# Kernel tuning notes

Measured on AMD Instinct MI355X. Metric: run time of the kernel, lower is better.

Reference implementation:

```python
import jax, jax.numpy as jnp
import numpy as np

WIN_H = WIN_W = 7
NUM_HEADS = 6
DIM = 192
HEAD_DIM = DIM // NUM_HEADS
NUM_WIN = 1024
B_ = 8192
N = WIN_H * WIN_W


def _relative_position_index(win_h, win_w):
    coords = np.stack(np.meshgrid(np.arange(win_h), np.arange(win_w), indexing='ij'))  # (2,h,w)
    flat = coords.reshape(2, -1)
    rel = flat[:, :, None] - flat[:, None, :]          # (2, N, N)
    rel = rel.transpose(1, 2, 0).astype(np.int32)      # (N, N, 2)
    rel[:, :, 0] += win_h - 1
    rel[:, :, 1] += win_w - 1
    rel[:, :, 0] *= 2 * win_w - 1
    return rel.sum(-1)                                 # (N, N) in [0, (2h-1)(2w-1))


def setup_inputs() -> dict:
    key = jax.random.key(0)
    ks = jax.random.split(key, 7)
    return {
        'x': jax.random.normal(ks[0], (B_, N, DIM), jnp.float32),
        'mask': jax.random.normal(ks[1], (NUM_WIN, N, N), jnp.float32),
        'qkv_w': jax.random.normal(ks[2], (3 * DIM, DIM), jnp.float32) * 0.02,
        'qkv_b': jax.random.normal(ks[3], (3 * DIM,), jnp.float32) * 0.02,
        'proj_w': jax.random.normal(ks[4], (DIM, DIM), jnp.float32) * 0.02,
        'proj_b': jax.random.normal(ks[5], (DIM,), jnp.float32) * 0.02,
        'rpb_table': jax.random.normal(ks[6], ((2 * WIN_H - 1) * (2 * WIN_W - 1), NUM_HEADS), jnp.float32) * 0.02,
        'rel_index': jnp.asarray(_relative_position_index(WIN_H, WIN_W)),
    }


def reference(x, mask, qkv_w, qkv_b, proj_w, proj_b, rpb_table, rel_index):
    B, n, C = x.shape
    H, hd = NUM_HEADS, HEAD_DIM
    scale = hd ** (-0.5)

    qkv = (x @ qkv_w.T + qkv_b).reshape(B, n, 3, H, hd)
    qkv = jnp.transpose(qkv, (2, 0, 3, 1, 4))          # (3, B, H, N, hd)
    q, k, v = qkv[0], qkv[1], qkv[2]

    attn = jnp.einsum('bhnd,bhmd->bhnm', q * scale, k)  # (B, H, N, N)

    # gathered relative position bias: (N*N,) -> (N, N, H) -> (H, N, N)
    bias = rpb_table[rel_index.reshape(-1)].reshape(n, n, H)
    attn = attn + jnp.transpose(bias, (2, 0, 1))[None]

    num_win = mask.shape[0]
    attn = attn.reshape(B // num_win, num_win, H, n, n) + mask[None, :, None]
    attn = jax.nn.softmax(attn, axis=-1).reshape(B, H, n, n)

    out = jnp.einsum('bhnm,bhmd->bhnd', attn, v)         # (B, H, N, hd)
    out = jnp.transpose(out, (0, 2, 1, 3)).reshape(B, n, H * hd)
    return out @ proj_w.T + proj_b
```

## Files before the change

### kernel.cpp

```cpp
#include <hip/hip_runtime.h>

#define NTOK  49
#define NWIN  1024
#define SCALE 0.17677669529663687f

#define SMEM_BYTES 102400

typedef __bf16 bfx8 __attribute__((ext_vector_type(8)));
typedef float  f32x4 __attribute__((ext_vector_type(4)));
typedef unsigned long long ull;
typedef unsigned int uint;

union BF8 { bfx8 v; ull q[2]; };
union BFU { __bf16 h[4]; ull q; };

__device__ __forceinline__ ull pack4(f32x4 a) {
    BFU u;
    u.h[0] = (__bf16)a[0]; u.h[1] = (__bf16)a[1];
    u.h[2] = (__bf16)a[2]; u.h[3] = (__bf16)a[3];
    return u.q;
}
__device__ __forceinline__ unsigned short f2bf(float f) {
    uint u = __builtin_bit_cast(uint, f);
    u += 0x7fffu + ((u >> 16) & 1u);
    return (unsigned short)(u >> 16);
}
__device__ __forceinline__ f32x4 mfma16(bfx8 a, bfx8 b, f32x4 c) {
    return __builtin_amdgcn_mfma_f32_16x16x32_bf16(a, b, c, 0, 0, 0);
}

extern "C" __global__ void wattn_prep(const float* __restrict__ qkv_w,
                                      const float* __restrict__ proj_w,
                                      const float* __restrict__ rpb,
                                      const int*   __restrict__ rel,
                                      const float* __restrict__ qkv_b,
                                      unsigned short* __restrict__ W1f,
                                      unsigned short* __restrict__ W2p,
                                      float* __restrict__ qkvbs,
                                      float* __restrict__ biasN)
{
    const int i = blockIdx.x * 256 + threadIdx.x;
    if (i < 110592) {
        const int e = i & 7, l = (i >> 3) & 63, f = i >> 9;
        const int kk = f % 6, oct = f / 6;
        const int R = oct * 16 + (l & 15), C = kk * 32 + (l >> 4) * 8 + e;
        float v = qkv_w[R * 192 + C];
        if (oct < 12) v *= SCALE;
        W1f[i] = f2bf(v);
    }
    if (i < 36864) {
        const int e = i & 7, l = (i >> 3) & 63, f = i >> 9;
        const int c2t = f / 6, H = f % 6;
        const int R = c2t * 16 + (l & 15);
        const int C = H * 32 + (e >> 2) * 16 + (l >> 4) * 4 + (e & 3);
        W2p[i] = f2bf(proj_w[R * 192 + C]);
    }
    if (i < 576) qkvbs[i] = (i < 192) ? qkv_b[i] * SCALE : qkv_b[i];
    if (i < 6 * NTOK * 64) {
        const int h = i / (NTOK * 64), ii = (i / 64) % NTOK, j = i % 64;
        biasN[i] = (j < NTOK) ? rpb[rel[ii * NTOK + j] * 6 + h] : -1e30f;
    }
}

extern "C" __global__ void __launch_bounds__(512, 2)
wattn_fused(const float* __restrict__ x,
            const float* __restrict__ mask,
            const float* __restrict__ proj_b,
            const unsigned short* __restrict__ W1f,
            const unsigned short* __restrict__ W2p,
            const float* __restrict__ qkvbs,
            const float* __restrict__ biasN,
            float* __restrict__ out)
{
    __shared__ char smem[SMEM_BYTES];
    char* const XB  = smem;
    char* const OBX = smem;
    char* const QBp = smem + 25600;
    char* const KBp = smem + 50176;
    char* const VTp = smem + 74752;

    const int tid  = threadIdx.x;
    const int wave = tid >> 6;
    const int lane = tid & 63;
    const int g    = lane >> 4;
    const int jn   = lane & 15;
    const int qt   = wave & 3;
    const int hh   = wave >> 2;
    const size_t b = blockIdx.x;

#pragma unroll
    for (int u = 0; u < 3; ++u) {
        const int i = tid + u * 512;
        if (i < 1500)
            *(uint*)(XB + (49 + i / 100) * 400 + (i % 100) * 4) = 0u;
    }
    {
        const float4* xw = (const float4*)(x + b * 9408);
#pragma unroll
        for (int u = 0; u < 5; ++u) {
            const int i = tid + u * 512;
            if (i < 2352) {
                float4 v = xw[i];
                f32x4 vv = {v.x, v.y, v.z, v.w};
                *(ull*)(XB + (i / 48) * 400 + (i % 48) * 8) = pack4(vv);
            }
        }
    }
    __syncthreads();

#pragma unroll
    for (int jj = 0; jj < 2; ++jj) {
        const int pr = wave + 8 * jj;
        const int octA = pr * 2;
        bfx8 wfA[6], wfB[6];
#pragma unroll
        for (int kk = 0; kk < 6; ++kk) {
            wfA[kk] = *(const bfx8*)(W1f + ((size_t)(octA * 6 + kk) * 64 + lane) * 8);
            wfB[kk] = *(const bfx8*)(W1f + ((size_t)((octA + 1) * 6 + kk) * 64 + lane) * 8);
        }
        if (pr < 12) {
            const f32x4 biA = *(const f32x4*)(qkvbs + octA * 16 + 4 * g);
            const f32x4 biB = *(const f32x4*)(qkvbs + (octA + 1) * 16 + 4 * g);
            char* const dst = (pr < 6) ? QBp : KBp;
            const int pp = (pr < 6) ? pr : pr - 6;
#pragma unroll
            for (int tt = 0; tt < 4; ++tt) {
                f32x4 aA = biA, aB = biB;
#pragma unroll
                for (int kk = 0; kk < 6; ++kk) {
                    bfx8 xf = *(const bfx8*)(XB + (tt * 16 + jn) * 400 + kk * 64 + g * 16);
                    aA = mfma16(wfA[kk], xf, aA);
                    aB = mfma16(wfB[kk], xf, aB);
                }
                BF8 o; o.q[0] = pack4(aA); o.q[1] = pack4(aB);
                *(bfx8*)(dst + ((tt * 6 + pp) * 64 + lane) * 16) = o.v;
            }
        } else {
            const float bvA = qkvbs[octA * 16 + jn];
            const float bvB = qkvbs[(octA + 1) * 16 + jn];
            const int cA = octA - 24;
#pragma unroll
            for (int tt = 0; tt < 4; ++tt) {
                f32x4 aA = {bvA, bvA, bvA, bvA};
                f32x4 aB = {bvB, bvB, bvB, bvB};
#pragma unroll
                for (int kk = 0; kk < 6; ++kk) {
                    bfx8 xf = *(const bfx8*)(XB + (tt * 16 + jn) * 400 + kk * 64 + g * 16);
                    aA = mfma16(xf, wfA[kk], aA);
                    aB = mfma16(xf, wfB[kk], aB);
                }
                const int voff = (tt >> 1) * 64 + g * 16 + (tt & 1) * 8;
                *(ull*)(VTp + (cA * 16 + jn) * 144 + voff)       = pack4(aA);
                *(ull*)(VTp + ((cA + 1) * 16 + jn) * 144 + voff) = pack4(aB);
            }
        }
    }
    {
        const int octA = 32 + (wave >> 2) * 2;
        const int tt = wave & 3;
        bfx8 wfA[6], wfB[6];
#pragma unroll
        for (int kk = 0; kk < 6; ++kk) {
            wfA[kk] = *(const bfx8*)(W1f + ((size_t)(octA * 6 + kk) * 64 + lane) * 8);
            wfB[kk] = *(const bfx8*)(W1f + ((size_t)((octA + 1) * 6 + kk) * 64 + lane) * 8);
        }
        const float bvA = qkvbs[octA * 16 + jn];
        const float bvB = qkvbs[(octA + 1) * 16 + jn];
        f32x4 aA = {bvA, bvA, bvA, bvA};
        f32x4 aB = {bvB, bvB, bvB, bvB};
#pragma unroll
        for (int kk = 0; kk < 6; ++kk) {
            bfx8 xf = *(const bfx8*)(XB + (tt * 16 + jn) * 400 + kk * 64 + g * 16);
            aA = mfma16(xf, wfA[kk], aA);
            aB = mfma16(xf, wfB[kk], aB);
        }
        const int cA = octA - 24;
        const int voff = (tt >> 1) * 64 + g * 16 + (tt & 1) * 8;
        *(ull*)(VTp + (cA * 16 + jn) * 144 + voff)       = pack4(aA);
        *(ull*)(VTp + ((cA + 1) * 16 + jn) * 144 + voff) = pack4(aB);
    }
    __syncthreads();

    const int iq = qt * 16 + jn;
    const int ic = iq < NTOK ? iq : NTOK - 1;
    const float* mw = mask + (b & (NWIN - 1)) * (NTOK * NTOK);
    float mv[4][4];
#pragma unroll
    for (int kt = 0; kt < 4; ++kt)
#pragma unroll
        for (int r = 0; r < 4; ++r) {
            const int j = kt * 16 + 4 * g + r;
            const int jc = j < NTOK ? j : NTOK - 1;
            mv[kt][r] = mw[ic * NTOK + jc];
        }

#pragma unroll
    for (int hl = 0; hl < 3; ++hl) {
        const int H = hh * 3 + hl;
        bfx8 qfr = *(const bfx8*)(QBp + ((qt * 6 + H) * 64 + lane) * 16);
        f32x4 p[4];
#pragma unroll
        for (int kt = 0; kt < 4; ++kt) {
            bfx8 kf = *(const bfx8*)(KBp + ((kt * 6 + H) * 64 + lane) * 16);
            f32x4 z = {0.f, 0.f, 0.f, 0.f};
            p[kt] = mfma16(kf, qfr, z);
        }
        float mx = -1e30f;
#pragma unroll
        for (int kt = 0; kt < 4; ++kt) {
            const f32x4 bm4 = *(const f32x4*)(biasN + ((size_t)H * NTOK + ic) * 64 + kt * 16 + 4 * g);
#pragma unroll
            for (int r = 0; r < 4; ++r) {
                const float v = p[kt][r] + bm4[r] + mv[kt][r];
                p[kt][r] = v;
                mx = fmaxf(mx, v);
            }
        }
        mx = fmaxf(mx, __shfl_xor(mx, 16));
        mx = fmaxf(mx, __shfl_xor(mx, 32));
        float sum = 0.f;
#pragma unroll
        for (int kt = 0; kt < 4; ++kt)
#pragma unroll
            for (int r = 0; r < 4; ++r) {
                p[kt][r] = __expf(p[kt][r] - mx);
                sum += p[kt][r];
            }
        sum += __shfl_xor(sum, 16);
        sum += __shfl_xor(sum, 32);
        const float inv = 1.f / sum;
        BF8 p01, p23;
        p01.q[0] = pack4(p[0]); p01.q[1] = pack4(p[1]);
        p23.q[0] = pack4(p[2]); p23.q[1] = pack4(p[3]);
#pragma unroll
        for (int ct = 0; ct < 2; ++ct) {
            const int row = H * 32 + ct * 16 + jn;
            bfx8 v0 = *(const bfx8*)(VTp + row * 144 + g * 16);
            bfx8 v1 = *(const bfx8*)(VTp + row * 144 + 64 + g * 16);
            f32x4 o = {0.f, 0.f, 0.f, 0.f};
            o = mfma16(v0, p01.v, o);
            o = mfma16(v1, p23.v, o);
            *(ull*)(OBX + ((qt * 6 + H) * 64 + lane) * 16 + ct * 8) = pack4(o * inv);
        }
    }
    __syncthreads();

    float* outp = out + b * 9408;
#pragma unroll
    for (int t = 0; t < 3; ++t) {
        const int j = wave + 8 * t;
        const int c2t = j >> 1;
        const int qh  = j & 1;
        bfx8 wf2[6];
#pragma unroll
        for (int H = 0; H < 6; ++H)
            wf2[H] = *(const bfx8*)(W2p + ((size_t)(c2t * 6 + H) * 64 + lane) * 8);
        const f32x4 pb = *(const f32x4*)(proj_b + c2t * 16 + 4 * g);
#pragma unroll
        for (int t2 = 0; t2 < 2; ++t2) {
            const int qt2 = qh * 2 + t2;
            f32x4 acc = pb;
#pragma unroll
            for (int H = 0; H < 6; ++H) {
                bfx8 ob = *(const bfx8*)(OBX + ((qt2 * 6 + H) * 64 + lane) * 16);
                acc = mfma16(wf2[H], ob, acc);
            }
            const int tok = qt2 * 16 + jn;
            if (tok < NTOK)
                *(f32x4*)(outp + tok * 192 + c2t * 16 + 4 * g) = acc;
        }
    }
}

extern "C" void kernel_launch(void* const* d_in, const int* in_sizes, int n_in,
                              void* d_out, int out_size, void* d_ws, size_t ws_size,
                              hipStream_t stream) {
    const float* x      = (const float*)d_in[0];
    const float* mask   = (const float*)d_in[1];
    const float* qkv_w  = (const float*)d_in[2];
    const float* qkv_b  = (const float*)d_in[3];
    const float* proj_w = (const float*)d_in[4];
    const float* proj_b = (const float*)d_in[5];
    const float* rpb    = (const float*)d_in[6];
    const int*   rel    = (const int*)d_in[7];
    float* outp = (float*)d_out;

    char* ws = (char*)d_ws;
    unsigned short* W1f = (unsigned short*)ws;
    unsigned short* W2p = (unsigned short*)(ws + 221184);
    float* qkvbs        = (float*)(ws + 221184 + 73728);
    float* biasN        = (float*)(ws + 221184 + 73728 + 2304);

    wattn_prep<<<432, 256, 0, stream>>>(qkv_w, proj_w, rpb, rel, qkv_b,
                                        W1f, W2p, qkvbs, biasN);
    wattn_fused<<<8192, 512, 0, stream>>>(x, mask, proj_b,
                                          W1f, W2p, qkvbs, biasN, outp);
}
```

Baseline: 427.9 us.

## Prefetch next-head Q/K/bias, fold bias+mask into MFMA accumulator, cache O fragments

Vectorizes the mask load and precombines bias plus mask as the initial accumulator of the QK^T MFMA, which removes the separate add pass. Loads of the Q, K and bias fragments for the next head are issued before the current head's softmax, so their latency overlaps compute. The projection stage now maps waves so each wave keeps a fixed token half, letting it load its O fragments from LDS once into registers and reuse them across all three output column tiles. The cost is higher register pressure, which may reduce occupancy.

```diff
diff --git a/kernel.cpp b/kernel.cpp
--- a/kernel.cpp
+++ b/kernel.cpp
@@ -184,38 +184,51 @@
     const int iq = qt * 16 + jn;
     const int ic = iq < NTOK ? iq : NTOK - 1;
     const float* mw = mask + (b & (NWIN - 1)) * (NTOK * NTOK);
-    float mv[4][4];
-#pragma unroll
-    for (int kt = 0; kt < 4; ++kt)
-#pragma unroll
-        for (int r = 0; r < 4; ++r) {
-            const int j = kt * 16 + 4 * g + r;
-            const int jc = j < NTOK ? j : NTOK - 1;
-            mv[kt][r] = mw[ic * NTOK + jc];
-        }
+    f32x4 mv4[4];
+#pragma unroll
+    for (int kt = 0; kt < 3; ++kt) {
+        float4 t;
+        __builtin_memcpy(&t, mw + ic * NTOK + kt * 16 + 4 * g, 16);
+        mv4[kt] = (f32x4){t.x, t.y, t.z, t.w};
+    }
+    {
+        const float m48 = mw[ic * NTOK + 48];
+        mv4[3] = (f32x4){m48, m48, m48, m48};
+    }
+
+    bfx8 qfr = *(const bfx8*)(QBp + ((qt * 6 + hh * 3) * 64 + lane) * 16);
+    bfx8 kfc[4];
+    f32x4 cic[4];
+#pragma unroll
+    for (int kt = 0; kt < 4; ++kt) {
+        kfc[kt] = *(const bfx8*)(KBp + ((kt * 6 + hh * 3) * 64 + lane) * 16);
+        const f32x4 bm4 = *(const f32x4*)(biasN + ((size_t)(hh * 3) * NTOK + ic) * 64 + kt * 16 + 4 * g);
+        cic[kt] = bm4 + mv4[kt];
+    }
 
 #pragma unroll
     for (int hl = 0; hl < 3; ++hl) {
         const int H = hh * 3 + hl;
-        bfx8 qfr = *(const bfx8*)(QBp + ((qt * 6 + H) * 64 + lane) * 16);
         f32x4 p[4];
 #pragma unroll
-        for (int kt = 0; kt < 4; ++kt) {
-            bfx8 kf = *(const bfx8*)(KBp + ((kt * 6 + H) * 64 + lane) * 16);
-            f32x4 z = {0.f, 0.f, 0.f, 0.f};
-            p[kt] = mfma16(kf, qfr, z);
+        for (int kt = 0; kt < 4; ++kt)
+            p[kt] = mfma16(kfc[kt], qfr, cic[kt]);
+        bfx8 qfn, kfn[4];
+        f32x4 cin[4];
+        if (hl < 2) {
+            qfn = *(const bfx8*)(QBp + ((qt * 6 + H + 1) * 64 + lane) * 16);
+#pragma unroll
+            for (int kt = 0; kt < 4; ++kt) {
+                kfn[kt] = *(const bfx8*)(KBp + ((kt * 6 + H + 1) * 64 + lane) * 16);
+                const f32x4 bm4 = *(const f32x4*)(biasN + ((size_t)(H + 1) * NTOK + ic) * 64 + kt * 16 + 4 * g);
+                cin[kt] = bm4 + mv4[kt];
+            }
         }
         float mx = -1e30f;
 #pragma unroll
-        for (int kt = 0; kt < 4; ++kt) {
-            const f32x4 bm4 = *(const f32x4*)(biasN + ((size_t)H * NTOK + ic) * 64 + kt * 16 + 4 * g);
-#pragma unroll
-            for (int r = 0; r < 4; ++r) {
-                const float v = p[kt][r] + bm4[r] + mv[kt][r];
-                p[kt][r] = v;
-                mx = fmaxf(mx, v);
-            }
-        }
+        for (int kt = 0; kt < 4; ++kt)
+#pragma unroll
+            for (int r = 0; r < 4; ++r) mx = fmaxf(mx, p[kt][r]);
         mx = fmaxf(mx, __shfl_xor(mx, 16));
         mx = fmaxf(mx, __shfl_xor(mx, 32));
         float sum = 0.f;
@@ -242,15 +255,26 @@
             o = mfma16(v1, p23.v, o);
             *(ull*)(OBX + ((qt * 6 + H) * 64 + lane) * 16 + ct * 8) = pack4(o * inv);
         }
+        if (hl < 2) {
+            qfr = qfn;
+#pragma unroll
+            for (int kt = 0; kt < 4; ++kt) { kfc[kt] = kfn[kt]; cic[kt] = cin[kt]; }
+        }
     }
     __syncthreads();
 
+    const int qh = wave & 1;
+    bfx8 obc[2][6];
+#pragma unroll
+    for (int t2 = 0; t2 < 2; ++t2)
+#pragma unroll
+        for (int H = 0; H < 6; ++H)
+            obc[t2][H] = *(const bfx8*)(OBX + (((qh * 2 + t2) * 6 + H) * 64 + lane) * 16);
+
     float* outp = out + b * 9408;
 #pragma unroll
     for (int t = 0; t < 3; ++t) {
-        const int j = wave + 8 * t;
-        const int c2t = j >> 1;
-        const int qh  = j & 1;
+        const int c2t = (wave >> 1) + 4 * t;
         bfx8 wf2[6];
 #pragma unroll
         for (int H = 0; H < 6; ++H)
@@ -261,10 +285,8 @@
             const int qt2 = qh * 2 + t2;
             f32x4 acc = pb;
 #pragma unroll
-            for (int H = 0; H < 6; ++H) {
-                bfx8 ob = *(const bfx8*)(OBX + ((qt2 * 6 + H) * 64 + lane) * 16);
-                acc = mfma16(wf2[H], ob, acc);
-            }
+            for (int H = 0; H < 6; ++H)
+                acc = mfma16(wf2[H], obc[t2][H], acc);
             const int tok = qt2 * 16 + jn;
             if (tok < NTOK)
                 *(f32x4*)(outp + tok * 192 + c2t * 16 + 4 * g) = acc;
```

New measurement: 420.0 us. About the same (-1.8%).
